# Performance work log

Hardware: AMD Instinct MI355X
Metric: run time of the kernel (lower is better)

The kernel has to match this reference:

```python
import jax, jax.numpy as jnp
import numpy as np

B, S, L, C = 256, 3, 4096, 2        # batch, num_slices, slice_length, in_channels
NN, CH, GH, HEADS = 4, 64, 64, 4    # num_nodes, cnn_hidden, gat_hidden, gat_heads
BD = CH * NN // 2                   # CNN branch_dim = 128
TD, TH, TL = 256, 4, 2              # transformer dim / heads / layers
NC = 5
DH = TD // TH


def setup_inputs():
    ks = iter(jax.random.split(jax.random.key(0), 128))
    def rn(shape, s=0.05):
        return jax.random.normal(next(ks), shape, jnp.float32) * s
    def bn(c):  # eval-mode BN params: gamma, beta, running_mean, running_var
        return (jax.random.uniform(next(ks), (2, c)) + 0.5, rn((2, c)),
                rn((2, c)), jax.random.uniform(next(ks), (2, c)) + 0.5)
    inp = {}
    inp['x_t'] = jax.random.normal(next(ks), (B, S, L, C), jnp.float32)
    inp['x_f'] = jax.random.uniform(next(ks), (B, S, L, C), jnp.float32)
    # dual-branch CNN params stacked on leading axis: [0]=time branch, [1]=freq branch
    inp['conv1_w'] = rn((2, 32, C, 15)); inp['conv1_b'] = rn((2, 32))
    inp['bn1_g'], inp['bn1_b'], inp['bn1_m'], inp['bn1_v'] = bn(32)
    inp['conv2_w'] = rn((2, 64, 32, 7)); inp['conv2_b'] = rn((2, 64))
    inp['bn2_g'], inp['bn2_b'], inp['bn2_m'], inp['bn2_v'] = bn(64)
    inp['conv3_w'] = rn((2, BD, 64, 3)); inp['conv3_b'] = rn((2, BD))
    inp['bn3_g'], inp['bn3_b'], inp['bn3_m'], inp['bn3_v'] = bn(BD)
    # PyG GATConv params (lin has no bias; att_src/att_dst per head; output bias)
    inp['gat_lin_w'] = rn((HEADS * GH, CH))
    inp['gat_att_src'] = rn((HEADS, GH)); inp['gat_att_dst'] = rn((HEADS, GH))
    inp['gat_bias'] = rn((HEADS * GH,))
    inp['feat_proj_w'] = rn((TD, NN * GH * HEADS)); inp['feat_proj_b'] = rn((TD,))
    # TransformerEncoder (post-norm, relu), params stacked over TL layers
    inp['tr_in_w'] = rn((TL, 3 * TD, TD)); inp['tr_in_b'] = rn((TL, 3 * TD))
    inp['tr_out_w'] = rn((TL, TD, TD)); inp['tr_out_b'] = rn((TL, TD))
    inp['tr_l1_w'] = rn((TL, 4 * TD, TD)); inp['tr_l1_b'] = rn((TL, 4 * TD))
    inp['tr_l2_w'] = rn((TL, TD, 4 * TD)); inp['tr_l2_b'] = rn((TL, TD))
    inp['tr_ln1_g'] = jnp.ones((TL, TD)); inp['tr_ln1_b'] = jnp.zeros((TL, TD))
    inp['tr_ln2_g'] = jnp.ones((TL, TD)); inp['tr_ln2_b'] = jnp.zeros((TL, TD))
    inp['ta_w'] = rn((1, TD)); inp['ta_b'] = rn((1,))
    inp['fc1_w'] = rn((128, TD)); inp['fc1_b'] = rn((128,))
    inp['fc2_w'] = rn((64, 128)); inp['fc2_b'] = rn((64,))
    inp['fc3_w'] = rn((NC, 64)); inp['fc3_b'] = rn((NC,))
    src = [i for i in range(NN) for j in range(NN) if i != j]
    dst = [j for i in range(NN) for j in range(NN) if i != j]
    inp['edge_index'] = jnp.array([src, dst], jnp.int32)
    return inp


def _conv_bn_relu(x, w, b, g, be, m, v, stride, pad):
    y = jax.lax.conv_general_dilated(x, w, (stride,), [(pad, pad)],
                                     dimension_numbers=('NCH', 'OIH', 'NCH'))
    y = (y + b[None, :, None] - m[None, :, None]) * (g / jnp.sqrt(v + 1e-5))[None, :, None] + be[None, :, None]
    return jax.nn.relu(y)


def _branch(x, c1w, c1b, g1, b1, m1, v1, c2w, c2b, g2, b2, m2, v2, c3w, c3b, g3, b3, m3, v3):
    y = _conv_bn_relu(x, c1w, c1b, g1, b1, m1, v1, 2, 7)
    y = _conv_bn_relu(y, c2w, c2b, g2, b2, m2, v2, 2, 3)
    y = _conv_bn_relu(y, c3w, c3b, g3, b3, m3, v3, 1, 1)
    return y.mean(axis=-1)  # AdaptiveAvgPool1d(1)


def _ln(x, g, b):
    mu = x.mean(-1, keepdims=True)
    var = ((x - mu) ** 2).mean(-1, keepdims=True)
    return (x - mu) / jnp.sqrt(var + 1e-5) * g + b


def _model(edge_index, x_t, x_f, conv1_w, conv1_b, bn1_g, bn1_b, bn1_m, bn1_v,
           conv2_w, conv2_b, bn2_g, bn2_b, bn2_m, bn2_v,
           conv3_w, conv3_b, bn3_g, bn3_b, bn3_m, bn3_v,
           gat_lin_w, gat_att_src, gat_att_dst, gat_bias,
           feat_proj_w, feat_proj_b,
           tr_in_w, tr_in_b, tr_out_w, tr_out_b, tr_l1_w, tr_l1_b, tr_l2_w, tr_l2_b,
           tr_ln1_g, tr_ln1_b, tr_ln2_g, tr_ln2_b,
           ta_w, ta_b, fc1_w, fc1_b, fc2_w, fc2_b, fc3_w, fc3_b):
    G = B * S  # fold (batch, slice) -> one big conv/GAT batch (replaces the python loops)
    xt = x_t.transpose(0, 1, 3, 2).reshape(G, C, L)
    xf = x_f.transpose(0, 1, 3, 2).reshape(G, C, L)
    xs = jnp.stack([xt, xf])  # [2, G, C, L]
    pooled = jax.vmap(_branch)(xs, conv1_w, conv1_b, bn1_g, bn1_b, bn1_m, bn1_v,
                               conv2_w, conv2_b, bn2_g, bn2_b, bn2_m, bn2_v,
                               conv3_w, conv3_b, bn3_g, bn3_b, bn3_m, bn3_v)  # [2, G, BD]
    feat = jnp.concatenate([pooled[0], pooled[1]], axis=1).reshape(G, NN, CH)
    # GATConv (dense over the tiny 4-node graph; softmax over in-edges per dest node)
    h = jnp.einsum('gnc,oc->gno', feat, gat_lin_w).reshape(G, NN, HEADS, GH)
    a_src = jnp.einsum('gnhd,hd->gnh', h, gat_att_src)
    a_dst = jnp.einsum('gnhd,hd->gnh', h, gat_att_dst)
    scores = jax.nn.leaky_relu(a_dst[:, :, None, :] + a_src[:, None, :, :], 0.2)  # [G,i,j,H]
    adj = jnp.zeros((NN, NN), bool).at[edge_index[1], edge_index[0]].set(True)
    adj = adj.at[jnp.arange(NN), jnp.arange(NN)].set(True)  # PyG adds self-loops
    alpha = jax.nn.softmax(jnp.where(adj[None, :, :, None], scores, -1e9), axis=2)
    gat_out = jnp.einsum('gijh,gjhd->gihd', alpha, h).reshape(G, NN, HEADS * GH) + gat_bias
    sl = gat_out.reshape(B, S, NN * HEADS * GH) @ feat_proj_w.T + feat_proj_b  # [B,S,TD]
    # positional encoding
    pos = jnp.arange(S, dtype=jnp.float32)[:, None]
    div = jnp.exp(jnp.arange(0, TD, 2, dtype=jnp.float32) * (-np.log(10000.0) / TD))
    pe = jnp.zeros((S, TD)).at[:, 0::2].set(jnp.sin(pos * div)).at[:, 1::2].set(jnp.cos(pos * div))
    x = sl + pe[None]
    # TransformerEncoder, post-norm, relu FFN
    for l in range(TL):
        qkv = x @ tr_in_w[l].T + tr_in_b[l]
        q, k, v = jnp.split(qkv, 3, axis=-1)
        q = q.reshape(B, S, TH, DH).transpose(0, 2, 1, 3)
        k = k.reshape(B, S, TH, DH).transpose(0, 2, 1, 3)
        v = v.reshape(B, S, TH, DH).transpose(0, 2, 1, 3)
        attn = jax.nn.softmax(jnp.einsum('bhqd,bhkd->bhqk', q, k) / np.sqrt(DH), axis=-1)
        a = jnp.einsum('bhqk,bhkd->bhqd', attn, v).transpose(0, 2, 1, 3).reshape(B, S, TD)
        a = a @ tr_out_w[l].T + tr_out_b[l]
        x = _ln(x + a, tr_ln1_g[l], tr_ln1_b[l])
        f = jax.nn.relu(x @ tr_l1_w[l].T + tr_l1_b[l]) @ tr_l2_w[l].T + tr_l2_b[l]
        x = _ln(x + f, tr_ln2_g[l], tr_ln2_b[l])
    w = jax.nn.softmax((x @ ta_w.T + ta_b)[..., 0], axis=1)  # [B,S] temporal attention
    ctx = jnp.einsum('bs,bsd->bd', w, x)
    o = jax.nn.relu(ctx @ fc1_w.T + fc1_b)
    o = jax.nn.relu(o @ fc2_w.T + fc2_b)
    return o @ fc3_w.T + fc3_b  # logits [B, NC]


def reference(x_t, x_f, conv1_w, conv1_b, bn1_g, bn1_b, bn1_m, bn1_v, conv2_w, conv2_b, bn2_g, bn2_b, bn2_m, bn2_v, conv3_w, conv3_b, bn3_g, bn3_b, bn3_m, bn3_v, gat_lin_w, gat_att_src, gat_att_dst, gat_bias, feat_proj_w, feat_proj_b, tr_in_w, tr_in_b, tr_out_w, tr_out_b, tr_l1_w, tr_l1_b, tr_l2_w, tr_l2_b, tr_ln1_g, tr_ln1_b, tr_ln2_g, tr_ln2_b, ta_w, ta_b, fc1_w, fc1_b, fc2_w, fc2_b, fc3_w, fc3_b, edge_index):
    return _model(edge_index, x_t, x_f, conv1_w, conv1_b, bn1_g, bn1_b, bn1_m, bn1_v,
                  conv2_w, conv2_b, bn2_g, bn2_b, bn2_m, bn2_v,
                  conv3_w, conv3_b, bn3_g, bn3_b, bn3_m, bn3_v,
                  gat_lin_w, gat_att_src, gat_att_dst, gat_bias,
                  feat_proj_w, feat_proj_b,
                  tr_in_w, tr_in_b, tr_out_w, tr_out_b, tr_l1_w, tr_l1_b, tr_l2_w, tr_l2_b,
                  tr_ln1_g, tr_ln1_b, tr_ln2_g, tr_ln2_b,
                  ta_w, ta_b, fc1_w, fc1_b, fc2_w, fc2_b, fc3_w, fc3_b)
```

## Files before the change

kernel.cpp:

```cpp
#include <hip/hip_runtime.h>
#include <math.h>

#define Bn 256
#define Sn 3
#define Ln 4096
#define Gn 768
#define TDn 256
#define TLn 2

#define WS_W1K   0
#define WS_W2K   1024
#define WS_W3K   15360
#define WS_H1    39936
#define WS_H2    40000
#define WS_H3    40128
#define WS_FPWH  40960
#define WS_INWH  172032
#define WS_OUTWH 368640
#define WS_L1WH  434176
#define WS_L2WH  696320
#define WS_POOL  958464
#define WS_XH    958464
#define WS_ABH   1056768
#define WS_SCR   1155072
#define WS_Y     1548288
#define WS_X     1744896

typedef _Float16 f16x8 __attribute__((ext_vector_type(8)));
typedef float f32x4 __attribute__((ext_vector_type(4)));
#define MFMA16(a,b,c) __builtin_amdgcn_mfma_f32_16x16x32_f16(a,b,c,0,0,0)

__global__ __launch_bounds__(256) void prep_kernel(
    const float* __restrict__ w1, const float* __restrict__ w2, const float* __restrict__ w3,
    const float* __restrict__ c1b, const float* __restrict__ g1, const float* __restrict__ b1,
    const float* __restrict__ m1, const float* __restrict__ v1,
    const float* __restrict__ c2b, const float* __restrict__ g2, const float* __restrict__ b2,
    const float* __restrict__ m2, const float* __restrict__ v2,
    const float* __restrict__ c3b, const float* __restrict__ g3, const float* __restrict__ b3,
    const float* __restrict__ m3, const float* __restrict__ v3,
    float* __restrict__ ws)
{
    int i = blockIdx.x * 256 + threadIdx.x;
    _Float16* w1k = (_Float16*)(ws + WS_W1K);
    _Float16* w2k = (_Float16*)(ws + WS_W2K);
    _Float16* w3k = (_Float16*)(ws + WS_W3K);
    if (i < 2048) {
        int k = i & 31, oc = (i >> 5) & 31, br = i >> 10;
        int c = k >> 4, tau = k & 15;
        int a = br * 32 + oc;
        float s = g1[a] / sqrtf(v1[a] + 1e-5f);
        float v = (tau < 15) ? w1[(((size_t)a * 2 + c) * 15) + tau] * s : 0.f;
        w1k[i] = (_Float16)v;
    }
    if (i < 28672) {
        int k = i % 224; int a = i / 224;
        int tblk = k >> 5, ic = k & 31;
        int t = (tblk < 4) ? 2 * tblk : 2 * (tblk - 4) + 1;
        float s = g2[a] / sqrtf(v2[a] + 1e-5f);
        w2k[i] = (_Float16)(w2[((size_t)a * 32 + ic) * 7 + t] * s);
    }
    if (i < 49152) {
        int k = i % 192; int a = i / 192;
        int t = k >> 6, ic = k & 63;
        float s = g3[a] / sqrtf(v3[a] + 1e-5f);
        w3k[i] = (_Float16)(w3[((size_t)a * 64 + ic) * 3 + t] * s);
    }
    if (i < 64)  { float s = g1[i] / sqrtf(v1[i] + 1e-5f); ws[WS_H1 + i] = (c1b[i] - m1[i]) * s + b1[i]; }
    if (i < 128) { float s = g2[i] / sqrtf(v2[i] + 1e-5f); ws[WS_H2 + i] = (c2b[i] - m2[i]) * s + b2[i]; }
    if (i < 256) { float s = g3[i] / sqrtf(v3[i] + 1e-5f); ws[WS_H3 + i] = (c3b[i] - m3[i]) * s + b3[i]; }
}

__global__ __launch_bounds__(256) void prep_tr_kernel(
    const float* __restrict__ fpw, const float* __restrict__ inw,
    const float* __restrict__ outw, const float* __restrict__ l1w,
    const float* __restrict__ l2w, float* __restrict__ ws)
{
    int i = blockIdx.x * 256 + threadIdx.x;
    _Float16* fpwh = (_Float16*)(ws + WS_FPWH);
    _Float16* inwh = (_Float16*)(ws + WS_INWH);
    _Float16* outwh = (_Float16*)(ws + WS_OUTWH);
    _Float16* l1wh = (_Float16*)(ws + WS_L1WH);
    _Float16* l2wh = (_Float16*)(ws + WS_L2WH);
    if (i < 262144) fpwh[i] = (_Float16)fpw[i];
    if (i < 393216) inwh[i] = (_Float16)inw[i];
    if (i < 131072) outwh[i] = (_Float16)outw[i];
    if (i < 524288) { l1wh[i] = (_Float16)l1w[i]; l2wh[i] = (_Float16)l2w[i]; }
}

__global__ __launch_bounds__(256, 2) void conv_mfma_kernel(
    const float* __restrict__ x_t, const float* __restrict__ x_f,
    const float* __restrict__ ws, float* __restrict__ pooled)
{
    __shared__ _Float16 xsf[2 * 576];
    __shared__ _Float16 y1[2][132 * 32];
    __shared__ _Float16 y2s[128 * 64];
    __shared__ float h1s[32];
    __shared__ float h2s[64];
    __shared__ float h3s[128];

    const int g = blockIdx.x, br = blockIdx.y;
    const int tid = threadIdx.x;
    const int lane = tid & 63, wv = tid >> 6;
    const int l15 = lane & 15, q4 = lane >> 4;

    const float* xin = (br == 0 ? x_t : x_f) + (size_t)g * (Ln * 2);
    const _Float16* w1k = (const _Float16*)(ws + WS_W1K) + br * 1024;
    const _Float16* w2k = (const _Float16*)(ws + WS_W2K) + br * 14336;
    const _Float16* w3k = (const _Float16*)(ws + WS_W3K) + br * 24576;

    if (tid < 32)  h1s[tid] = ws[WS_H1 + br * 32 + tid];
    if (tid < 64)  h2s[tid] = ws[WS_H2 + br * 64 + tid];
    if (tid < 128) h3s[tid] = ws[WS_H3 + br * 128 + tid];

    f16x8 a1[2];
    #pragma unroll
    for (int mt = 0; mt < 2; ++mt)
        a1[mt] = *(const f16x8*)(w1k + (mt * 16 + l15) * 32 + q4 * 8);

    const int mg = wv & 1, ng = wv >> 1;

    const _Float16* w2row = w2k + (size_t)l15 * 224 + q4 * 8;
    const _Float16* w3row = w3k + (size_t)(mg * 64 + l15) * 192 + q4 * 8;

    float pool_[4][4];
    #pragma unroll
    for (int mt = 0; mt < 4; ++mt)
        #pragma unroll
        for (int r = 0; r < 4; ++r) pool_[mt][r] = 0.f;

    const f32x4 vzero = {0.f, 0.f, 0.f, 0.f};

    for (int tile = 0; tile < 9; ++tile) {
        const int P0 = tile * 126;
        const int Q0 = 2 * P0 - 5;
        const int x0 = 4 * P0 - 17;

        for (int l = tid; l < 576; l += 256) {
            int xl = x0 + l;
            float a = 0.f, b = 0.f;
            if (xl >= 0 && xl < Ln) { float2 v = *(const float2*)(xin + (size_t)xl * 2); a = v.x; b = v.y; }
            xsf[l] = (_Float16)a; xsf[576 + l] = (_Float16)b;
        }
        __syncthreads();

        const uint* xsu = (const uint*)xsf;
        for (int nt = wv; nt < 17; nt += 4) {
            int j0 = nt * 16 + l15;
            union { f16x8 v; uint u[4]; } bf;
            int ubase = (q4 >> 1) * 288 + j0 + (q4 & 1) * 4;
            #pragma unroll
            for (int ii = 0; ii < 4; ++ii) bf.u[ii] = xsu[ubase + ii];
            f32x4 c1acc[2] = {vzero, vzero};
            c1acc[0] = MFMA16(a1[0], bf.v, c1acc[0]);
            c1acc[1] = MFMA16(a1[1], bf.v, c1acc[1]);

            if (j0 <= 260) {
                int q = Q0 + j0;
                bool val = (q >= 0) && (q < 2048);
                int i = j0 >> 1, par = j0 & 1;
                #pragma unroll
                for (int mt = 0; mt < 2; ++mt) {
                    int oc0 = mt * 16 + q4 * 4;
                    union { _Float16 h[4]; uint2 u; } pk;
                    #pragma unroll
                    for (int r = 0; r < 4; ++r) {
                        float y = c1acc[mt][r] + h1s[oc0 + r];
                        y = y > 0.f ? y : 0.f;
                        pk.h[r] = val ? (_Float16)y : (_Float16)0.f;
                    }
                    int gq = mt * 2 + (q4 >> 1), sub = q4 & 1;
                    *(uint2*)(&y1[par][(i * 4 + (gq ^ (i & 3))) * 8 + sub * 4]) = pk.u;
                }
            }
        }
        __syncthreads();

        {
            f32x4 c2[4][2];
            #pragma unroll
            for (int mt = 0; mt < 4; ++mt) { c2[mt][0] = vzero; c2[mt][1] = vzero; }
            f16x8 a2c[4];
            #pragma unroll
            for (int mt = 0; mt < 4; ++mt)
                a2c[mt] = *(const f16x8*)(w2row + (size_t)mt * 16 * 224);
            #pragma unroll 1
            for (int ks = 0; ks < 7; ++ks) {
                int roff = (ks < 4) ? ks : ks - 4;
                const _Float16* yb = y1[(ks < 4) ? 0 : 1];
                f16x8 bb[2];
                #pragma unroll
                for (int jj = 0; jj < 2; ++jj) {
                    int n = wv * 32 + jj * 16 + l15;
                    int i = n + roff;
                    bb[jj] = *(const f16x8*)(yb + (i * 4 + (q4 ^ (i & 3))) * 8);
                }
                f16x8 a2n[4];
                if (ks < 6) {
                    #pragma unroll
                    for (int mt = 0; mt < 4; ++mt)
                        a2n[mt] = *(const f16x8*)(w2row + (size_t)mt * 16 * 224 + (ks + 1) * 32);
                }
                #pragma unroll
                for (int mt = 0; mt < 4; ++mt) {
                    c2[mt][0] = MFMA16(a2c[mt], bb[0], c2[mt][0]);
                    c2[mt][1] = MFMA16(a2c[mt], bb[1], c2[mt][1]);
                }
                if (ks < 6) {
                    #pragma unroll
                    for (int mt = 0; mt < 4; ++mt) a2c[mt] = a2n[mt];
                }
            }
            #pragma unroll
            for (int jj = 0; jj < 2; ++jj) {
                int n = wv * 32 + jj * 16 + l15;
                int p2 = P0 - 1 + n;
                bool val = (p2 >= 0) && (p2 < 1024);
                #pragma unroll
                for (int mt = 0; mt < 4; ++mt) {
                    int oc0 = mt * 16 + q4 * 4;
                    union { _Float16 h[4]; uint2 u; } pk;
                    #pragma unroll
                    for (int r = 0; r < 4; ++r) {
                        float y = c2[mt][jj][r] + h2s[oc0 + r];
                        y = y > 0.f ? y : 0.f;
                        pk.h[r] = val ? (_Float16)y : (_Float16)0.f;
                    }
                    int gq = oc0 >> 3, sub = q4 & 1;
                    *(uint2*)(&y2s[(n * 8 + (gq ^ (n & 7))) * 8 + sub * 4]) = pk.u;
                }
            }
        }
        __syncthreads();

        #pragma unroll 1
        for (int half = 0; half < 2; ++half) {
            f32x4 c3[4][2];
            #pragma unroll
            for (int mt = 0; mt < 4; ++mt) { c3[mt][0] = vzero; c3[mt][1] = vzero; }
            f16x8 a3c[4];
            #pragma unroll
            for (int mt = 0; mt < 4; ++mt)
                a3c[mt] = *(const f16x8*)(w3row + (size_t)mt * 16 * 192);
            #pragma unroll 1
            for (int ks = 0; ks < 6; ++ks) {
                int t = ks >> 1, ich = ks & 1;
                f16x8 b3[2];
                #pragma unroll
                for (int jj = 0; jj < 2; ++jj) {
                    int np = ng * 64 + (half * 2 + jj) * 16 + l15;
                    int r = np + t; r = r < 128 ? r : 127;
                    int gq3 = ich * 4 + q4;
                    b3[jj] = *(const f16x8*)(&y2s[(r * 8 + (gq3 ^ (r & 7))) * 8]);
                }
                f16x8 a3n[4];
                if (ks < 5) {
                    #pragma unroll
                    for (int mt = 0; mt < 4; ++mt)
                        a3n[mt] = *(const f16x8*)(w3row + (size_t)mt * 16 * 192 + (ks + 1) * 32);
                }
                #pragma unroll
                for (int mt = 0; mt < 4; ++mt) {
                    c3[mt][0] = MFMA16(a3c[mt], b3[0], c3[mt][0]);
                    c3[mt][1] = MFMA16(a3c[mt], b3[1], c3[mt][1]);
                }
                if (ks < 5) {
                    #pragma unroll
                    for (int mt = 0; mt < 4; ++mt) a3c[mt] = a3n[mt];
                }
            }
            #pragma unroll
            for (int mt = 0; mt < 4; ++mt) {
                int oc0 = mg * 64 + mt * 16 + q4 * 4;
                #pragma unroll
                for (int jj = 0; jj < 2; ++jj) {
                    int np = ng * 64 + (half * 2 + jj) * 16 + l15;
                    int p3 = P0 + np;
                    bool val = (np < 126) && (p3 < 1024);
                    #pragma unroll
                    for (int r = 0; r < 4; ++r) {
                        float y = c3[mt][jj][r] + h3s[oc0 + r];
                        y = y > 0.f ? y : 0.f;
                        pool_[mt][r] += val ? y : 0.f;
                    }
                }
            }
        }
        __syncthreads();
    }

    float* pout = pooled + g * 256 + br * 128;
    #pragma unroll
    for (int mt = 0; mt < 4; ++mt)
        #pragma unroll
        for (int r = 0; r < 4; ++r) {
            float v = pool_[mt][r];
            v += __shfl_xor(v, 1, 64);
            v += __shfl_xor(v, 2, 64);
            v += __shfl_xor(v, 4, 64);
            v += __shfl_xor(v, 8, 64);
            if (l15 == 0) {
                int oc = mg * 64 + mt * 16 + q4 * 4 + r;
                atomicAdd(&pout[oc], v * (1.f / 1024.f));
            }
        }
}

__global__ __launch_bounds__(256) void gat_kernel(
    const float* __restrict__ glw, const float* __restrict__ att_src,
    const float* __restrict__ att_dst, const float* __restrict__ gbias,
    const float* __restrict__ pooled, _Float16* __restrict__ gouth)
{
    __shared__ float feats[256];
    __shared__ float hs[4 * 256];
    __shared__ float av[32];
    __shared__ float alpha[64];

    int g = blockIdx.x, tid = threadIdx.x;
    feats[tid] = pooled[g * 256 + tid];
    __syncthreads();

    {
        int o = tid;
        const float* w = glw + o * 64;
        float a0 = 0, a1 = 0, a2 = 0, a3 = 0;
        for (int c = 0; c < 64; ++c) {
            float wvv = w[c];
            a0 = fmaf(feats[c],       wvv, a0);
            a1 = fmaf(feats[64 + c],  wvv, a1);
            a2 = fmaf(feats[128 + c], wvv, a2);
            a3 = fmaf(feats[192 + c], wvv, a3);
        }
        hs[o] = a0; hs[256 + o] = a1; hs[512 + o] = a2; hs[768 + o] = a3;
    }
    __syncthreads();

    if (tid < 32) {
        int n = (tid & 15) >> 2, hd = tid & 3;
        const float* aw = (tid < 16) ? att_src : att_dst;
        float s = 0;
        for (int d = 0; d < 64; ++d) s = fmaf(hs[n * 256 + hd * 64 + d], aw[hd * 64 + d], s);
        av[tid] = s;
    }
    __syncthreads();

    if (tid < 16) {
        int i = tid >> 2, hd = tid & 3;
        float sc[4], mx = -1e30f;
        #pragma unroll
        for (int j = 0; j < 4; ++j) {
            float v = av[16 + i * 4 + hd] + av[j * 4 + hd];
            v = v > 0.f ? v : 0.2f * v;
            sc[j] = v; mx = fmaxf(mx, v);
        }
        float den = 0;
        #pragma unroll
        for (int j = 0; j < 4; ++j) { sc[j] = expf(sc[j] - mx); den += sc[j]; }
        #pragma unroll
        for (int j = 0; j < 4; ++j) alpha[(i * 4 + j) * 4 + hd] = sc[j] / den;
    }
    __syncthreads();

    {
        int o = tid, hd = o >> 6;
        #pragma unroll
        for (int i = 0; i < 4; ++i) {
            float acc = gbias[o];
            #pragma unroll
            for (int j = 0; j < 4; ++j) acc = fmaf(alpha[(i * 4 + j) * 4 + hd], hs[j * 256 + o], acc);
            gouth[(size_t)g * 1024 + i * 256 + o] = (_Float16)acc;
        }
    }
}

template <int K, int MODE>
__global__ __launch_bounds__(256) void mfma_gemm_kernel(
    const _Float16* __restrict__ A, const _Float16* __restrict__ W,
    const float* __restrict__ bias, float* __restrict__ out32,
    _Float16* __restrict__ out16, int N)
{
    const int tid = threadIdx.x;
    const int wv = tid >> 6, l15 = tid & 15, q4 = (tid & 63) >> 4;
    const int m0 = blockIdx.x * 64 + wv * 16;
    const int n0 = blockIdx.y * 64;

    const f32x4 vzero = {0.f, 0.f, 0.f, 0.f};
    f32x4 acc[4] = {vzero, vzero, vzero, vzero};

    const _Float16* arow = A + (size_t)(m0 + l15) * K + q4 * 8;
    #pragma unroll 4
    for (int ks = 0; ks < K / 32; ++ks) {
        f16x8 a = *(const f16x8*)(arow + ks * 32);
        #pragma unroll
        for (int nt = 0; nt < 4; ++nt) {
            f16x8 b = *(const f16x8*)(W + (size_t)(n0 + nt * 16 + l15) * K + ks * 32 + q4 * 8);
            acc[nt] = MFMA16(a, b, acc[nt]);
        }
    }

    #pragma unroll
    for (int nt = 0; nt < 4; ++nt) {
        int n = n0 + nt * 16 + l15;
        float bs = bias[n];
        #pragma unroll
        for (int r = 0; r < 4; ++r) {
            int m = m0 + q4 * 4 + r;
            float v = acc[nt][r] + bs;
            if (MODE == 1) v = fmaxf(v, 0.f);
            if (MODE == 3) {
                int s = m % 3;
                int kk = n >> 1;
                float dv = expf((float)kk * -0.07195588f);
                float arg = (float)s * dv;
                v += (n & 1) ? cosf(arg) : sinf(arg);
            }
            if (MODE == 0 || MODE == 3) out32[(size_t)m * N + n] = v;
            if (MODE == 1 || MODE == 3) out16[(size_t)m * N + n] = (_Float16)v;
        }
    }
}

__global__ __launch_bounds__(256) void res_ln_kernel(
    const float* __restrict__ Y, const float* __restrict__ res,
    const float* __restrict__ gamma, const float* __restrict__ beta,
    float* __restrict__ X, _Float16* __restrict__ XH)
{
    __shared__ float ys[8][256];
    __shared__ float red[8][2];
    int r0 = blockIdx.x * 8, tid = threadIdx.x;
    #pragma unroll
    for (int r = 0; r < 8; ++r)
        ys[r][tid] = Y[(size_t)(r0 + r) * 256 + tid] + res[(size_t)(r0 + r) * 256 + tid];
    __syncthreads();
    {
        int r = tid >> 5, l = tid & 31;
        float s = 0, s2 = 0;
        for (int c = l; c < 256; c += 32) { float v = ys[r][c]; s += v; s2 += v * v; }
        #pragma unroll
        for (int m = 16; m > 0; m >>= 1) { s += __shfl_xor(s, m, 32); s2 += __shfl_xor(s2, m, 32); }
        if (l == 0) {
            float mu = s * (1.f / 256.f);
            float var = s2 * (1.f / 256.f) - mu * mu;
            red[r][0] = mu; red[r][1] = 1.0f / sqrtf(var + 1e-5f);
        }
    }
    __syncthreads();
    #pragma unroll
    for (int r = 0; r < 8; ++r) {
        float v = (ys[r][tid] - red[r][0]) * red[r][1] * gamma[tid] + beta[tid];
        X[(size_t)(r0 + r) * 256 + tid] = v;
        XH[(size_t)(r0 + r) * 256 + tid] = (_Float16)v;
    }
}

__global__ __launch_bounds__(256) void attn_kernel(
    const float* __restrict__ qkv, _Float16* __restrict__ abufh)
{
    int b = blockIdx.x, tid = threadIdx.x, head = tid >> 6, d = tid & 63;
    const float* base = qkv + (size_t)b * 3 * 768 + head * 64 + d;
    float q[3], k[3], v[3];
    #pragma unroll
    for (int s = 0; s < 3; ++s) {
        const float* row = base + s * 768;
        q[s] = row[0]; k[s] = row[256]; v[s] = row[512];
    }
    float sc[3][3];
    #pragma unroll
    for (int si = 0; si < 3; ++si)
        #pragma unroll
        for (int sj = 0; sj < 3; ++sj) {
            float p = q[si] * k[sj];
            #pragma unroll
            for (int m = 32; m > 0; m >>= 1) p += __shfl_xor(p, m, 64);
            sc[si][sj] = p * 0.125f;
        }
    #pragma unroll
    for (int si = 0; si < 3; ++si) {
        float mx = fmaxf(sc[si][0], fmaxf(sc[si][1], sc[si][2]));
        float e0 = expf(sc[si][0] - mx), e1 = expf(sc[si][1] - mx), e2 = expf(sc[si][2] - mx);
        float den = e0 + e1 + e2;
        float o = (e0 * v[0] + e1 * v[1] + e2 * v[2]) / den;
        abufh[(size_t)(b * 3 + si) * 256 + head * 64 + d] = (_Float16)o;
    }
}

__global__ __launch_bounds__(256) void head_kernel(
    const float* __restrict__ X, const float* __restrict__ taw, const float* __restrict__ tab,
    const float* __restrict__ f1w, const float* __restrict__ f1b,
    const float* __restrict__ f2w, const float* __restrict__ f2b,
    const float* __restrict__ f3w, const float* __restrict__ f3b,
    float* __restrict__ out)
{
    __shared__ float xs[3 * 256];
    __shared__ float wsm[3];
    __shared__ float cs[256];
    __shared__ float a1[128];
    __shared__ float a2[64];
    int b = blockIdx.x, tid = threadIdx.x;
    for (int idx = tid; idx < 768; idx += 256) xs[idx] = X[(size_t)b * 768 + idx];
    __syncthreads();
    if (tid < 3) {
        float s = tab[0];
        for (int d = 0; d < 256; ++d) s = fmaf(xs[tid * 256 + d], taw[d], s);
        wsm[tid] = s;
    }
    __syncthreads();
    {
        float m = fmaxf(wsm[0], fmaxf(wsm[1], wsm[2]));
        float e0 = expf(wsm[0] - m), e1 = expf(wsm[1] - m), e2 = expf(wsm[2] - m);
        float den = e0 + e1 + e2;
        cs[tid] = (e0 * xs[tid] + e1 * xs[256 + tid] + e2 * xs[512 + tid]) / den;
    }
    __syncthreads();
    if (tid < 128) {
        float a = f1b[tid];
        const float* w = f1w + tid * 256;
        for (int c = 0; c < 256; ++c) a = fmaf(cs[c], w[c], a);
        a1[tid] = fmaxf(a, 0.f);
    }
    __syncthreads();
    if (tid < 64) {
        float a = f2b[tid];
        const float* w = f2w + tid * 128;
        for (int c = 0; c < 128; ++c) a = fmaf(a1[c], w[c], a);
        a2[tid] = fmaxf(a, 0.f);
    }
    __syncthreads();
    if (tid < 5) {
        float a = f3b[tid];
        const float* w = f3w + tid * 64;
        for (int c = 0; c < 64; ++c) a = fmaf(a2[c], w[c], a);
        out[b * 5 + tid] = a;
    }
}

extern "C" void kernel_launch(void* const* d_in, const int* in_sizes, int n_in,
                              void* d_out, int out_size, void* d_ws, size_t ws_size,
                              hipStream_t stream) {
    const float* x_t     = (const float*)d_in[0];
    const float* x_f     = (const float*)d_in[1];
    const float* conv1_w = (const float*)d_in[2];
    const float* conv1_b = (const float*)d_in[3];
    const float* bn1_g   = (const float*)d_in[4];
    const float* bn1_b   = (const float*)d_in[5];
    const float* bn1_m   = (const float*)d_in[6];
    const float* bn1_v   = (const float*)d_in[7];
    const float* conv2_w = (const float*)d_in[8];
    const float* conv2_b = (const float*)d_in[9];
    const float* bn2_g   = (const float*)d_in[10];
    const float* bn2_b   = (const float*)d_in[11];
    const float* bn2_m   = (const float*)d_in[12];
    const float* bn2_v   = (const float*)d_in[13];
    const float* conv3_w = (const float*)d_in[14];
    const float* conv3_b = (const float*)d_in[15];
    const float* bn3_g   = (const float*)d_in[16];
    const float* bn3_b   = (const float*)d_in[17];
    const float* bn3_m   = (const float*)d_in[18];
    const float* bn3_v   = (const float*)d_in[19];
    const float* gat_lin_w   = (const float*)d_in[20];
    const float* gat_att_src = (const float*)d_in[21];
    const float* gat_att_dst = (const float*)d_in[22];
    const float* gat_bias    = (const float*)d_in[23];
    const float* feat_proj_w = (const float*)d_in[24];
    const float* feat_proj_b = (const float*)d_in[25];
    const float* tr_in_w  = (const float*)d_in[26];
    const float* tr_in_b  = (const float*)d_in[27];
    const float* tr_out_w = (const float*)d_in[28];
    const float* tr_out_b = (const float*)d_in[29];
    const float* tr_l1_w  = (const float*)d_in[30];
    const float* tr_l1_b  = (const float*)d_in[31];
    const float* tr_l2_w  = (const float*)d_in[32];
    const float* tr_l2_b  = (const float*)d_in[33];
    const float* tr_ln1_g = (const float*)d_in[34];
    const float* tr_ln1_b = (const float*)d_in[35];
    const float* tr_ln2_g = (const float*)d_in[36];
    const float* tr_ln2_b = (const float*)d_in[37];
    const float* ta_w  = (const float*)d_in[38];
    const float* ta_b  = (const float*)d_in[39];
    const float* fc1_w = (const float*)d_in[40];
    const float* fc1_b = (const float*)d_in[41];
    const float* fc2_w = (const float*)d_in[42];
    const float* fc2_b = (const float*)d_in[43];
    const float* fc3_w = (const float*)d_in[44];
    const float* fc3_b = (const float*)d_in[45];

    float* ws    = (float*)d_ws;
    float* POOL  = ws + WS_POOL;
    float* X     = ws + WS_X;
    float* QKV   = ws + WS_SCR;
    float* Y     = ws + WS_Y;
    _Float16* GOUTH = (_Float16*)(ws + WS_SCR);
    _Float16* MIDH  = (_Float16*)(ws + WS_SCR);
    _Float16* XH    = (_Float16*)(ws + WS_XH);
    _Float16* ABH   = (_Float16*)(ws + WS_ABH);
    const _Float16* FPWH  = (const _Float16*)(ws + WS_FPWH);
    const _Float16* INWH  = (const _Float16*)(ws + WS_INWH);
    const _Float16* OUTWH = (const _Float16*)(ws + WS_OUTWH);
    const _Float16* L1WH  = (const _Float16*)(ws + WS_L1WH);
    const _Float16* L2WH  = (const _Float16*)(ws + WS_L2WH);
    float* out = (float*)d_out;

    hipMemsetAsync(POOL, 0, (size_t)Gn * 256 * sizeof(float), stream);

    prep_kernel<<<192, 256, 0, stream>>>(conv1_w, conv2_w, conv3_w,
        conv1_b, bn1_g, bn1_b, bn1_m, bn1_v,
        conv2_b, bn2_g, bn2_b, bn2_m, bn2_v,
        conv3_b, bn3_g, bn3_b, bn3_m, bn3_v, ws);
    prep_tr_kernel<<<2048, 256, 0, stream>>>(feat_proj_w, tr_in_w, tr_out_w,
                                             tr_l1_w, tr_l2_w, ws);

    conv_mfma_kernel<<<dim3(Gn, 2), 256, 0, stream>>>(x_t, x_f, ws, POOL);

    gat_kernel<<<Gn, 256, 0, stream>>>(gat_lin_w, gat_att_src, gat_att_dst, gat_bias,
                                       POOL, GOUTH);

    mfma_gemm_kernel<1024, 3><<<dim3(12, 4), 256, 0, stream>>>(
        GOUTH, FPWH, feat_proj_b, X, XH, 256);

    for (int l = 0; l < TLn; ++l) {
        mfma_gemm_kernel<256, 0><<<dim3(12, 12), 256, 0, stream>>>(
            XH, INWH + (size_t)l * 196608, tr_in_b + l * 768, QKV, nullptr, 768);
        attn_kernel<<<Bn, 256, 0, stream>>>(QKV, ABH);
        mfma_gemm_kernel<256, 0><<<dim3(12, 4), 256, 0, stream>>>(
            ABH, OUTWH + (size_t)l * 65536, tr_out_b + l * 256, Y, nullptr, 256);
        res_ln_kernel<<<Gn / 8, 256, 0, stream>>>(
            Y, X, tr_ln1_g + l * 256, tr_ln1_b + l * 256, X, XH);
        mfma_gemm_kernel<256, 1><<<dim3(12, 16), 256, 0, stream>>>(
            XH, L1WH + (size_t)l * 262144, tr_l1_b + l * 1024, nullptr, MIDH, 1024);
        mfma_gemm_kernel<1024, 0><<<dim3(12, 4), 256, 0, stream>>>(
            MIDH, L2WH + (size_t)l * 262144, tr_l2_b + l * 256, Y, nullptr, 256);
        res_ln_kernel<<<Gn / 8, 256, 0, stream>>>(
            Y, X, tr_ln2_g + l * 256, tr_ln2_b + l * 256, X, XH);
    }

    head_kernel<<<Bn, 256, 0, stream>>>(X, ta_w, ta_b, fc1_w, fc1_b,
                                        fc2_w, fc2_b, fc3_w, fc3_b, out);
}
```

Before: 722.6 us.

## Raise conv kernel occupancy, pool in LDS, fuse residual-LayerNorm into GEMM

The conv kernel now targets 4 waves per SIMD instead of 2. To fit that register budget it splits the conv2 accumulation into a non-unrolled loop over column halves and keeps loops rolled. Pooled sums are reduced in shared memory and written once per block, which removes the global memset and the global atomics. The out-projection and FFN2 GEMMs are fused with the residual add and LayerNorm in a new 16-row-tile kernel, dropping the intermediate Y buffer and two launches per layer. The fused GEMM uses only 48 blocks with direct global loads, so it may underuse the GPU compared with the tiled GEMM.

```diff
diff --git a/kernel.cpp b/kernel.cpp
--- a/kernel.cpp
+++ b/kernel.cpp
@@ -87,7 +87,7 @@
     if (i < 524288) { l1wh[i] = (_Float16)l1w[i]; l2wh[i] = (_Float16)l2w[i]; }
 }
 
-__global__ __launch_bounds__(256, 2) void conv_mfma_kernel(
+__global__ __launch_bounds__(256, 4) void conv_mfma_kernel(
     const float* __restrict__ x_t, const float* __restrict__ x_f,
     const float* __restrict__ ws, float* __restrict__ pooled)
 {
@@ -97,6 +97,7 @@
     __shared__ float h1s[32];
     __shared__ float h2s[64];
     __shared__ float h3s[128];
+    __shared__ float pbuf[128];
 
     const int g = blockIdx.x, br = blockIdx.y;
     const int tid = threadIdx.x;
@@ -110,7 +111,7 @@
 
     if (tid < 32)  h1s[tid] = ws[WS_H1 + br * 32 + tid];
     if (tid < 64)  h2s[tid] = ws[WS_H2 + br * 64 + tid];
-    if (tid < 128) h3s[tid] = ws[WS_H3 + br * 128 + tid];
+    if (tid < 128) { h3s[tid] = ws[WS_H3 + br * 128 + tid]; pbuf[tid] = 0.f; }
 
     f16x8 a1[2];
     #pragma unroll
@@ -130,6 +131,7 @@
 
     const f32x4 vzero = {0.f, 0.f, 0.f, 0.f};
 
+    #pragma unroll 1
     for (int tile = 0; tile < 9; ++tile) {
         const int P0 = tile * 126;
         const int Q0 = 2 * P0 - 5;
@@ -144,6 +146,7 @@
         __syncthreads();
 
         const uint* xsu = (const uint*)xsf;
+        #pragma unroll 1
         for (int nt = wv; nt < 17; nt += 4) {
             int j0 = nt * 16 + l15;
             union { f16x8 v; uint u[4]; } bf;
@@ -175,25 +178,20 @@
         }
         __syncthreads();
 
-        {
-            f32x4 c2[4][2];
-            #pragma unroll
-            for (int mt = 0; mt < 4; ++mt) { c2[mt][0] = vzero; c2[mt][1] = vzero; }
+        #pragma unroll 1
+        for (int jj = 0; jj < 2; ++jj) {
+            f32x4 c2[4] = {vzero, vzero, vzero, vzero};
             f16x8 a2c[4];
             #pragma unroll
             for (int mt = 0; mt < 4; ++mt)
                 a2c[mt] = *(const f16x8*)(w2row + (size_t)mt * 16 * 224);
+            const int n = wv * 32 + jj * 16 + l15;
             #pragma unroll 1
             for (int ks = 0; ks < 7; ++ks) {
                 int roff = (ks < 4) ? ks : ks - 4;
                 const _Float16* yb = y1[(ks < 4) ? 0 : 1];
-                f16x8 bb[2];
-                #pragma unroll
-                for (int jj = 0; jj < 2; ++jj) {
-                    int n = wv * 32 + jj * 16 + l15;
-                    int i = n + roff;
-                    bb[jj] = *(const f16x8*)(yb + (i * 4 + (q4 ^ (i & 3))) * 8);
-                }
+                int i = n + roff;
+                f16x8 bb = *(const f16x8*)(yb + (i * 4 + (q4 ^ (i & 3))) * 8);
                 f16x8 a2n[4];
                 if (ks < 6) {
                     #pragma unroll
@@ -201,33 +199,27 @@
                         a2n[mt] = *(const f16x8*)(w2row + (size_t)mt * 16 * 224 + (ks + 1) * 32);
                 }
                 #pragma unroll
-                for (int mt = 0; mt < 4; ++mt) {
-                    c2[mt][0] = MFMA16(a2c[mt], bb[0], c2[mt][0]);
-                    c2[mt][1] = MFMA16(a2c[mt], bb[1], c2[mt][1]);
-                }
+                for (int mt = 0; mt < 4; ++mt)
+                    c2[mt] = MFMA16(a2c[mt], bb, c2[mt]);
                 if (ks < 6) {
                     #pragma unroll
                     for (int mt = 0; mt < 4; ++mt) a2c[mt] = a2n[mt];
                 }
             }
-            #pragma unroll
-            for (int jj = 0; jj < 2; ++jj) {
-                int n = wv * 32 + jj * 16 + l15;
-                int p2 = P0 - 1 + n;
-                bool val = (p2 >= 0) && (p2 < 1024);
+            int p2 = P0 - 1 + n;
+            bool val = (p2 >= 0) && (p2 < 1024);
+            #pragma unroll
+            for (int mt = 0; mt < 4; ++mt) {
+                int oc0 = mt * 16 + q4 * 4;
+                union { _Float16 h[4]; uint2 u; } pk;
                 #pragma unroll
-                for (int mt = 0; mt < 4; ++mt) {
-                    int oc0 = mt * 16 + q4 * 4;
-                    union { _Float16 h[4]; uint2 u; } pk;
-                    #pragma unroll
-                    for (int r = 0; r < 4; ++r) {
-                        float y = c2[mt][jj][r] + h2s[oc0 + r];
-                        y = y > 0.f ? y : 0.f;
-                        pk.h[r] = val ? (_Float16)y : (_Float16)0.f;
-                    }
-                    int gq = oc0 >> 3, sub = q4 & 1;
-                    *(uint2*)(&y2s[(n * 8 + (gq ^ (n & 7))) * 8 + sub * 4]) = pk.u;
-                }
+                for (int r = 0; r < 4; ++r) {
+                    float y = c2[mt][r] + h2s[oc0 + r];
+                    y = y > 0.f ? y : 0.f;
+                    pk.h[r] = val ? (_Float16)y : (_Float16)0.f;
+                }
+                int gq = oc0 >> 3, sub = q4 & 1;
+                *(uint2*)(&y2s[(n * 8 + (gq ^ (n & 7))) * 8 + sub * 4]) = pk.u;
             }
         }
         __syncthreads();
@@ -275,12 +267,12 @@
                 for (int jj = 0; jj < 2; ++jj) {
                     int np = ng * 64 + (half * 2 + jj) * 16 + l15;
                     int p3 = P0 + np;
-                    bool val = (np < 126) && (p3 < 1024);
+                    float valf = ((np < 126) && (p3 < 1024)) ? 1.f : 0.f;
                     #pragma unroll
                     for (int r = 0; r < 4; ++r) {
                         float y = c3[mt][jj][r] + h3s[oc0 + r];
                         y = y > 0.f ? y : 0.f;
-                        pool_[mt][r] += val ? y : 0.f;
+                        pool_[mt][r] = fmaf(y, valf, pool_[mt][r]);
                     }
                 }
             }
@@ -288,7 +280,6 @@
         __syncthreads();
     }
 
-    float* pout = pooled + g * 256 + br * 128;
     #pragma unroll
     for (int mt = 0; mt < 4; ++mt)
         #pragma unroll
@@ -298,11 +289,10 @@
             v += __shfl_xor(v, 2, 64);
             v += __shfl_xor(v, 4, 64);
             v += __shfl_xor(v, 8, 64);
-            if (l15 == 0) {
-                int oc = mg * 64 + mt * 16 + q4 * 4 + r;
-                atomicAdd(&pout[oc], v * (1.f / 1024.f));
-            }
-        }
+            if (l15 == 0) atomicAdd(&pbuf[mg * 64 + mt * 16 + q4 * 4 + r], v);
+        }
+    __syncthreads();
+    if (tid < 128) pooled[g * 256 + br * 128 + tid] = pbuf[tid] * (1.f / 1024.f);
 }
 
 __global__ __launch_bounds__(256) void gat_kernel(
@@ -419,36 +409,66 @@
     }
 }
 
-__global__ __launch_bounds__(256) void res_ln_kernel(
-    const float* __restrict__ Y, const float* __restrict__ res,
+template <int K>
+__global__ __launch_bounds__(256) void gemm_ln_kernel(
+    const _Float16* __restrict__ A, const _Float16* __restrict__ W,
+    const float* __restrict__ bias,
     const float* __restrict__ gamma, const float* __restrict__ beta,
     float* __restrict__ X, _Float16* __restrict__ XH)
 {
-    __shared__ float ys[8][256];
-    __shared__ float red[8][2];
-    int r0 = blockIdx.x * 8, tid = threadIdx.x;
-    #pragma unroll
-    for (int r = 0; r < 8; ++r)
-        ys[r][tid] = Y[(size_t)(r0 + r) * 256 + tid] + res[(size_t)(r0 + r) * 256 + tid];
-    __syncthreads();
+    __shared__ float ys[16][260];
+    const int tid = threadIdx.x;
+    const int wv = tid >> 6, l15 = tid & 15, q4 = (tid & 63) >> 4;
+    const int r0 = blockIdx.x * 16;
+    const int n0 = wv * 64;
+
+    const f32x4 vzero = {0.f, 0.f, 0.f, 0.f};
+    f32x4 acc[4] = {vzero, vzero, vzero, vzero};
+
+    const _Float16* arow = A + (size_t)(r0 + l15) * K + q4 * 8;
+    #pragma unroll 4
+    for (int ks = 0; ks < K / 32; ++ks) {
+        f16x8 a = *(const f16x8*)(arow + ks * 32);
+        #pragma unroll
+        for (int nt = 0; nt < 4; ++nt) {
+            f16x8 b = *(const f16x8*)(W + (size_t)(n0 + nt * 16 + l15) * K + ks * 32 + q4 * 8);
+            acc[nt] = MFMA16(a, b, acc[nt]);
+        }
+    }
+
+    #pragma unroll
+    for (int nt = 0; nt < 4; ++nt) {
+        int col = n0 + nt * 16 + l15;
+        float bs = bias[col];
+        #pragma unroll
+        for (int r = 0; r < 4; ++r) {
+            int rowl = q4 * 4 + r;
+            ys[rowl][col] = acc[nt][r] + bs + X[(size_t)(r0 + rowl) * 256 + col];
+        }
+    }
+    __syncthreads();
+
     {
-        int r = tid >> 5, l = tid & 31;
+        int row = tid >> 4, l16 = tid & 15;
         float s = 0, s2 = 0;
-        for (int c = l; c < 256; c += 32) { float v = ys[r][c]; s += v; s2 += v * v; }
-        #pragma unroll
-        for (int m = 16; m > 0; m >>= 1) { s += __shfl_xor(s, m, 32); s2 += __shfl_xor(s2, m, 32); }
-        if (l == 0) {
-            float mu = s * (1.f / 256.f);
-            float var = s2 * (1.f / 256.f) - mu * mu;
-            red[r][0] = mu; red[r][1] = 1.0f / sqrtf(var + 1e-5f);
-        }
-    }
-    __syncthreads();
-    #pragma unroll
-    for (int r = 0; r < 8; ++r) {
-        float v = (ys[r][tid] - red[r][0]) * red[r][1] * gamma[tid] + beta[tid];
-        X[(size_t)(r0 + r) * 256 + tid] = v;
-        XH[(size_t)(r0 + r) * 256 + tid] = (_Float16)v;
+        #pragma unroll
+        for (int c0 = 0; c0 < 256; c0 += 16) {
+            float v = ys[row][c0 + l16]; s += v; s2 += v * v;
+        }
+        s += __shfl_xor(s, 1, 64);  s2 += __shfl_xor(s2, 1, 64);
+        s += __shfl_xor(s, 2, 64);  s2 += __shfl_xor(s2, 2, 64);
+        s += __shfl_xor(s, 4, 64);  s2 += __shfl_xor(s2, 4, 64);
+        s += __shfl_xor(s, 8, 64);  s2 += __shfl_xor(s2, 8, 64);
+        float mu = s * (1.f / 256.f);
+        float var = s2 * (1.f / 256.f) - mu * mu;
+        float inv = 1.0f / sqrtf(var + 1e-5f);
+        #pragma unroll
+        for (int c0 = 0; c0 < 256; c0 += 16) {
+            int c = c0 + l16;
+            float v = (ys[row][c] - mu) * inv * gamma[c] + beta[c];
+            X[(size_t)(r0 + row) * 256 + c] = v;
+            XH[(size_t)(r0 + row) * 256 + c] = (_Float16)v;
+        }
     }
 }
 
@@ -587,7 +607,6 @@
     float* POOL  = ws + WS_POOL;
     float* X     = ws + WS_X;
     float* QKV   = ws + WS_SCR;
-    float* Y     = ws + WS_Y;
     _Float16* GOUTH = (_Float16*)(ws + WS_SCR);
     _Float16* MIDH  = (_Float16*)(ws + WS_SCR);
     _Float16* XH    = (_Float16*)(ws + WS_XH);
@@ -599,8 +618,6 @@
     const _Float16* L2WH  = (const _Float16*)(ws + WS_L2WH);
     float* out = (float*)d_out;
 
-    hipMemsetAsync(POOL, 0, (size_t)Gn * 256 * sizeof(float), stream);
-
     prep_kernel<<<192, 256, 0, stream>>>(conv1_w, conv2_w, conv3_w,
         conv1_b, bn1_g, bn1_b, bn1_m, bn1_v,
         conv2_b, bn2_g, bn2_b, bn2_m, bn2_v,
@@ -620,16 +637,14 @@
         mfma_gemm_kernel<256, 0><<<dim3(12, 12), 256, 0, stream>>>(
             XH, INWH + (size_t)l * 196608, tr_in_b + l * 768, QKV, nullptr, 768);
         attn_kernel<<<Bn, 256, 0, stream>>>(QKV, ABH);
-        mfma_gemm_kernel<256, 0><<<dim3(12, 4), 256, 0, stream>>>(
-            ABH, OUTWH + (size_t)l * 65536, tr_out_b + l * 256, Y, nullptr, 256);
-        res_ln_kernel<<<Gn / 8, 256, 0, stream>>>(
-            Y, X, tr_ln1_g + l * 256, tr_ln1_b + l * 256, X, XH);
+        gemm_ln_kernel<256><<<48, 256, 0, stream>>>(
+            ABH, OUTWH + (size_t)l * 65536, tr_out_b + l * 256,
+            tr_ln1_g + l * 256, tr_ln1_b + l * 256, X, XH);
         mfma_gemm_kernel<256, 1><<<dim3(12, 16), 256, 0, stream>>>(
             XH, L1WH + (size_t)l * 262144, tr_l1_b + l * 1024, nullptr, MIDH, 1024);
-        mfma_gemm_kernel<1024, 0><<<dim3(12, 4), 256, 0, stream>>>(
-            MIDH, L2WH + (size_t)l * 262144, tr_l2_b + l * 256, Y, nullptr, 256);
-        res_ln_kernel<<<Gn / 8, 256, 0, stream>>>(
-            Y, X, tr_ln2_g + l * 256, tr_ln2_b + l * 256, X, XH);
+        gemm_ln_kernel<1024><<<48, 256, 0, stream>>>(
+            MIDH, L2WH + (size_t)l * 262144, tr_l2_b + l * 256,
+            tr_ln2_g + l * 256, tr_ln2_b + l * 256, X, XH);
     }
 
     head_kernel<<<Bn, 256, 0, stream>>>(X, ta_w, ta_b, fc1_w, fc1_b,
```

After: 883.0 us. 1.22x slower.
